# Kernel optimization log

Hardware: AMD Instinct MI355X
Metric: run time of the kernel (lower is better)

The kernel has to match this reference:

```python
import jax, jax.numpy as jnp
import numpy as np

E = 8        # n_experts
H = 1024     # hidden
F = 1024     # ffn intermediate
K = 2        # top_k
B, T = 2, 1024


def setup_inputs() -> dict:
    key = jax.random.key(0)
    k1, k2, k3, k4 = jax.random.split(key, 4)
    return {
        "hidden_states": jax.random.normal(k1, (B, T, H), dtype=jnp.float32),
        "router_weight": jax.random.normal(k2, (E, H), dtype=jnp.float32),
        "gate_up_proj": jax.random.normal(k3, (E, 2 * F, H), dtype=jnp.float32),
        "down_proj": jax.random.normal(k4, (E, H, F), dtype=jnp.float32),
    }


def reference(hidden_states, router_weight, gate_up_proj, down_proj):
    b, t, h_dim = hidden_states.shape
    h = hidden_states.reshape(-1, h_dim)                      # [N, H]

    # Router: logits -> softmax -> top-k -> renormalize (matches FakeFusedRouter)
    logits = h @ router_weight.T                              # [N, E]
    probs = jax.nn.softmax(logits, axis=-1)
    top_v, top_i = jax.lax.top_k(probs, K)                    # [N, K]
    top_v = top_v / top_v.sum(axis=-1, keepdims=True)

    # Combine weights per expert: w[e, n] = sum_k top_v[n,k] * [top_i[n,k]==e]
    combine = (jax.nn.one_hot(top_i, E, dtype=top_v.dtype) * top_v[..., None]).sum(axis=1)  # [N, E]
    combine = combine.T                                       # [E, N]

    # Scan over experts: each expert runs its SwiGLU FFN over all tokens,
    # masked/weighted by combine (zero weight == token not routed there).
    def body(acc, xs):
        gu, dp, w = xs                                        # [2F,H], [H,F], [N]
        gate, up = jnp.split(h @ gu.T, 2, axis=-1)            # [N,F] each
        out = (jax.nn.silu(gate) * up) @ dp.T                 # [N,H]
        return acc + w[:, None] * out, None

    acc0 = jnp.zeros_like(h)
    final, _ = jax.lax.scan(body, acc0, (gate_up_proj, down_proj, combine))
    return final.reshape(b, t, h_dim)
```

## Files before the change

kernel.cpp:

```cpp
#include <hip/hip_runtime.h>


#define NTOK   2048
#define HDIM   1024
#define FDIM   1024
#define NEXP   8
#define NKROWS 4096
#define MAXTILES 40

typedef __attribute__((ext_vector_type(8))) __bf16 bf16x8;
typedef __attribute__((ext_vector_type(4))) float  floatx4;

__device__ __forceinline__ unsigned short f2bf(float x) {
    unsigned int u = __builtin_bit_cast(unsigned int, x);
    u += 0x7FFFu + ((u >> 16) & 1u);
    return (unsigned short)(u >> 16);
}

__device__ __forceinline__ float bf2f(unsigned short v) {
    unsigned int u = (unsigned int)v << 16;
    return __builtin_bit_cast(float, u);
}

__device__ __forceinline__ uint4 pack8(float4 a, float4 b) {
    uint4 o;
    o.x = (unsigned)f2bf(a.x) | ((unsigned)f2bf(a.y) << 16);
    o.y = (unsigned)f2bf(a.z) | ((unsigned)f2bf(a.w) << 16);
    o.z = (unsigned)f2bf(b.x) | ((unsigned)f2bf(b.y) << 16);
    o.w = (unsigned)f2bf(b.z) | ((unsigned)f2bf(b.w) << 16);
    return o;
}

__device__ __forceinline__ void dma16(const void* g, void* l) {
    __builtin_amdgcn_global_load_lds(
        (const __attribute__((address_space(1))) unsigned int*)g,
        (__attribute__((address_space(3))) unsigned int*)l, 16, 0, 0);
}

__global__ __launch_bounds__(256) void k_convert_w(
    const float* __restrict__ gu, const float* __restrict__ dp,
    unsigned short* __restrict__ gubf, unsigned short* __restrict__ dpbf)
{
    int b = blockIdx.x;
    const float* src;
    unsigned short* dst;
    size_t base;
    if (b < 8192) { base = (size_t)b * 2048;          src = gu; dst = gubf; }
    else          { base = (size_t)(b - 8192) * 2048; src = dp; dst = dpbf; }
    size_t i = base + (size_t)threadIdx.x * 8;
    const float4* s = reinterpret_cast<const float4*>(src + i);
    float4 a = s[0], c = s[1];
    *reinterpret_cast<uint4*>(dst + i) = pack8(a, c);
}

__global__ __launch_bounds__(256) void k_router(
    const float* __restrict__ h, const float* __restrict__ rw,
    unsigned short* __restrict__ hbf,
    int* __restrict__ topk_idx, float* __restrict__ topk_w)
{
    const int lane = threadIdx.x & 63;
    const int wave = threadIdx.x >> 6;
    const int n = blockIdx.x * 4 + wave;

    const float4* hp = reinterpret_cast<const float4*>(h + (size_t)n * HDIM);
    uint2* hb = reinterpret_cast<uint2*>(hbf + (size_t)n * HDIM);
    float acc[NEXP];
#pragma unroll
    for (int e = 0; e < NEXP; ++e) acc[e] = 0.f;

#pragma unroll
    for (int i0 = 0; i0 < HDIM / 4; i0 += 64) {
        float4 hv = hp[i0 + lane];
        uint2 o;
        o.x = (unsigned)f2bf(hv.x) | ((unsigned)f2bf(hv.y) << 16);
        o.y = (unsigned)f2bf(hv.z) | ((unsigned)f2bf(hv.w) << 16);
        hb[i0 + lane] = o;
#pragma unroll
        for (int e = 0; e < NEXP; ++e) {
            float4 rv = reinterpret_cast<const float4*>(rw + e * HDIM)[i0 + lane];
            acc[e] += hv.x * rv.x + hv.y * rv.y + hv.z * rv.z + hv.w * rv.w;
        }
    }
#pragma unroll
    for (int e = 0; e < NEXP; ++e) {
#pragma unroll
        for (int off = 32; off > 0; off >>= 1)
            acc[e] += __shfl_xor(acc[e], off);
    }
    if (lane == 0) {
        int i0 = 0; float m0 = acc[0];
        for (int e = 1; e < NEXP; ++e) if (acc[e] > m0) { m0 = acc[e]; i0 = e; }
        int i1 = -1; float m1 = -3.0e38f;
        for (int e = 0; e < NEXP; ++e) if (e != i0 && acc[e] > m1) { m1 = acc[e]; i1 = e; }
        float d  = __expf(m1 - m0);
        float w0 = 1.f / (1.f + d);
        topk_idx[n * 2 + 0] = i0;
        topk_idx[n * 2 + 1] = i1;
        topk_w [n * 2 + 0] = w0;
        topk_w [n * 2 + 1] = 1.f - w0;
    }
}

__global__ __launch_bounds__(256) void k_build_perm(
    const int* __restrict__ topk_idx, const float* __restrict__ topk_w,
    int* __restrict__ offsets, int* __restrict__ perm_slot, float* __restrict__ row_w,
    int* __restrict__ tile_e, int* __restrict__ tile_rt)
{
    __shared__ int cnt[NEXP];
    __shared__ int cur[NEXP];
    __shared__ int off[NEXP + 1];
    const int t = threadIdx.x;
    if (t < NEXP) cnt[t] = 0;
    __syncthreads();
    for (int s = t; s < NKROWS; s += 256) atomicAdd(&cnt[topk_idx[s]], 1);
    __syncthreads();
    if (t == 0) {
        int a = 0;
        for (int e = 0; e < NEXP; ++e) { off[e] = a; a += cnt[e]; cur[e] = off[e]; }
        off[NEXP] = a;
        int nt = 0;
        for (int e = 0; e < NEXP; ++e) {
            int ne = cnt[e];
            for (int r = 0; r * 128 < ne; ++r) { tile_e[nt] = e; tile_rt[nt] = r; ++nt; }
        }
        for (; nt < MAXTILES; ++nt) { tile_e[nt] = -1; tile_rt[nt] = 0; }
    }
    __syncthreads();
    for (int s = t; s < NKROWS; s += 256) {
        int e = topk_idx[s];
        int pos = atomicAdd(&cur[e], 1);
        perm_slot[pos] = s;
        row_w[pos] = topk_w[s];
    }
    if (t < NEXP + 1) offsets[t] = off[t];
}

__global__ __launch_bounds__(256, 2) void k_gemm1(
    const unsigned short* __restrict__ hbf, const unsigned short* __restrict__ gubf,
    const int* __restrict__ offsets, const int* __restrict__ perm_slot,
    const int* __restrict__ tile_e, const int* __restrict__ tile_rt,
    unsigned short* __restrict__ act)
{
    const int e = tile_e[blockIdx.y];
    if (e < 0) return;
    const int rt = tile_rt[blockIdx.y];
    const int off_e = offsets[e];
    const int n_e   = offsets[e + 1] - off_e;
    const int p0 = off_e + rt * 128;
    const int nr = min(128, n_e - rt * 128);
    const int c0 = blockIdx.x * 64;

    __shared__ __align__(16) char smA [2][128 * 128];
    __shared__ __align__(16) char smBg[2][64 * 128];
    __shared__ __align__(16) char smBu[2][64 * 128];
    __shared__ int sTok[128];

    const int t = threadIdx.x;
    const int lane = t & 63;
    const int wv = t >> 6;
    const int wr = wv >> 1, wc = wv & 1;
    if (t < 128) sTok[t] = perm_slot[min(p0 + t, NKROWS - 1)] >> 1;
    __syncthreads();

    const int rin = lane >> 3;
    const int pre = ((lane & 7) << 4) ^ (rin << 4);

    const char* asrc[4];
    int aldo[4];
#pragma unroll
    for (int c = 0; c < 4; ++c) {
        int ch = wv * 4 + c;
        int row = ch * 8 + rin;
        asrc[c] = (const char*)(hbf + (size_t)sTok[row] * HDIM) + pre;
        aldo[c] = ch * 1024;
    }
    const unsigned short* guE = gubf + (size_t)e * (2 * FDIM) * HDIM;
    const char* gsrc[2];
    const char* usrc[2];
    int bldo[2];
#pragma unroll
    for (int c = 0; c < 2; ++c) {
        int ch = wv * 2 + c;
        int col = ch * 8 + rin;
        gsrc[c] = (const char*)(guE + (size_t)(c0 + col) * HDIM) + pre;
        usrc[c] = (const char*)(guE + (size_t)(FDIM + c0 + col) * HDIM) + pre;
        bldo[c] = ch * 1024;
    }

    floatx4 accg[4][2], accu[4][2];
#pragma unroll
    for (int m = 0; m < 4; ++m)
#pragma unroll
        for (int nn = 0; nn < 2; ++nn) { accg[m][nn] = (floatx4)0.f; accu[m][nn] = (floatx4)0.f; }

#define STAGE1(k0, buf)                                                         \
    {                                                                           \
        _Pragma("unroll")                                                       \
        for (int c = 0; c < 4; ++c) dma16(asrc[c] + (size_t)(k0) * 2, smA [buf] + aldo[c]); \
        _Pragma("unroll")                                                       \
        for (int c = 0; c < 2; ++c) dma16(gsrc[c] + (size_t)(k0) * 2, smBg[buf] + bldo[c]); \
        _Pragma("unroll")                                                       \
        for (int c = 0; c < 2; ++c) dma16(usrc[c] + (size_t)(k0) * 2, smBu[buf] + bldo[c]); \
    }

    STAGE1(0, 0);
    STAGE1(64, 1);

    for (int step = 0; step < 16; ++step) {
        if (step < 15) asm volatile("s_waitcnt vmcnt(8)" ::: "memory");
        else           asm volatile("s_waitcnt vmcnt(0)" ::: "memory");
        __builtin_amdgcn_s_barrier();
        __builtin_amdgcn_sched_barrier(0);
        const int cur = step & 1;
#pragma unroll
        for (int kk = 0; kk < 2; ++kk) {
            const int kA = kk * 64 + (lane >> 4) * 16;
            bf16x8 a[4], fg[2], fu[2];
#pragma unroll
            for (int m = 0; m < 4; ++m) {
                int row = wr * 64 + m * 16 + (lane & 15);
                a[m] = *reinterpret_cast<const bf16x8*>(&smA[cur][row * 128 + (kA ^ ((row & 7) << 4))]);
            }
#pragma unroll
            for (int nn = 0; nn < 2; ++nn) {
                int cc = wc * 32 + nn * 16 + (lane & 15);
                int ad = cc * 128 + (kA ^ ((cc & 7) << 4));
                fg[nn] = *reinterpret_cast<const bf16x8*>(&smBg[cur][ad]);
                fu[nn] = *reinterpret_cast<const bf16x8*>(&smBu[cur][ad]);
            }
#pragma unroll
            for (int m = 0; m < 4; ++m)
#pragma unroll
                for (int nn = 0; nn < 2; ++nn) {
                    accg[m][nn] = __builtin_amdgcn_mfma_f32_16x16x32_bf16(a[m], fg[nn], accg[m][nn], 0, 0, 0);
                    accu[m][nn] = __builtin_amdgcn_mfma_f32_16x16x32_bf16(a[m], fu[nn], accu[m][nn], 0, 0, 0);
                }
        }
        __builtin_amdgcn_sched_barrier(0);
        __builtin_amdgcn_s_barrier();
        if (step < 14) STAGE1((step + 2) * 64, cur);
    }
#undef STAGE1

#pragma unroll
    for (int m = 0; m < 4; ++m)
#pragma unroll
        for (int nn = 0; nn < 2; ++nn)
#pragma unroll
            for (int j = 0; j < 4; ++j) {
                int rr = wr * 64 + m * 16 + ((lane >> 4) << 2) + j;
                if (rr < nr) {
                    int f = c0 + wc * 32 + nn * 16 + (lane & 15);
                    float gg = accg[m][nn][j];
                    float uu = accu[m][nn][j];
                    float s = gg / (1.f + __expf(-gg));
                    act[(size_t)(p0 + rr) * FDIM + f] = f2bf(s * uu);
                }
            }
}

__global__ __launch_bounds__(256, 2) void k_gemm2(
    const unsigned short* __restrict__ act, const unsigned short* __restrict__ dpbf,
    const int* __restrict__ offsets, const int* __restrict__ perm_slot,
    const int* __restrict__ tile_e, const int* __restrict__ tile_rt,
    const float* __restrict__ row_w, unsigned short* __restrict__ partial)
{
    const int e = tile_e[blockIdx.y];
    if (e < 0) return;
    const int rt = tile_rt[blockIdx.y];
    const int off_e = offsets[e];
    const int n_e   = offsets[e + 1] - off_e;
    const int p0 = off_e + rt * 128;
    const int nr = min(128, n_e - rt * 128);
    const int c0 = blockIdx.x * 128;

    __shared__ __align__(16) char smA[2][128 * 128];
    __shared__ __align__(16) char smB[2][128 * 128];
    __shared__ int   sSlot[128];
    __shared__ float sW[128];

    const int t = threadIdx.x;
    const int lane = t & 63;
    const int wv = t >> 6;
    const int wr = wv >> 1, wc = wv & 1;
    if (t < 128) {
        int p = min(p0 + t, NKROWS - 1);
        sSlot[t] = perm_slot[p];
        sW[t]    = row_w[p];
    }
    __syncthreads();

    const int rin = lane >> 3;
    const int pre = ((lane & 7) << 4) ^ (rin << 4);

    const char* asrc[4];
    int aldo[4];
#pragma unroll
    for (int c = 0; c < 4; ++c) {
        int ch = wv * 4 + c;
        int row = ch * 8 + rin;
        int p = min(p0 + row, NKROWS - 1);
        asrc[c] = (const char*)(act + (size_t)p * FDIM) + pre;
        aldo[c] = ch * 1024;
    }
    const unsigned short* dpE = dpbf + (size_t)e * HDIM * FDIM;
    const char* bsrc[4];
    int bldo[4];
#pragma unroll
    for (int c = 0; c < 4; ++c) {
        int ch = wv * 4 + c;
        int col = ch * 8 + rin;
        bsrc[c] = (const char*)(dpE + (size_t)(c0 + col) * FDIM) + pre;
        bldo[c] = ch * 1024;
    }

    floatx4 acc[4][4];
#pragma unroll
    for (int m = 0; m < 4; ++m)
#pragma unroll
        for (int nn = 0; nn < 4; ++nn) acc[m][nn] = (floatx4)0.f;

#define STAGE2(k0, buf)                                                         \
    {                                                                           \
        _Pragma("unroll")                                                       \
        for (int c = 0; c < 4; ++c) dma16(asrc[c] + (size_t)(k0) * 2, smA[buf] + aldo[c]); \
        _Pragma("unroll")                                                       \
        for (int c = 0; c < 4; ++c) dma16(bsrc[c] + (size_t)(k0) * 2, smB[buf] + bldo[c]); \
    }

    STAGE2(0, 0);
    STAGE2(64, 1);

    for (int step = 0; step < 16; ++step) {
        if (step < 15) asm volatile("s_waitcnt vmcnt(8)" ::: "memory");
        else           asm volatile("s_waitcnt vmcnt(0)" ::: "memory");
        __builtin_amdgcn_s_barrier();
        __builtin_amdgcn_sched_barrier(0);
        const int cur = step & 1;
#pragma unroll
        for (int kk = 0; kk < 2; ++kk) {
            const int kA = kk * 64 + (lane >> 4) * 16;
            bf16x8 a[4], fb[4];
#pragma unroll
            for (int m = 0; m < 4; ++m) {
                int row = wr * 64 + m * 16 + (lane & 15);
                a[m] = *reinterpret_cast<const bf16x8*>(&smA[cur][row * 128 + (kA ^ ((row & 7) << 4))]);
            }
#pragma unroll
            for (int nn = 0; nn < 4; ++nn) {
                int cc = wc * 64 + nn * 16 + (lane & 15);
                fb[nn] = *reinterpret_cast<const bf16x8*>(&smB[cur][cc * 128 + (kA ^ ((cc & 7) << 4))]);
            }
#pragma unroll
            for (int m = 0; m < 4; ++m)
#pragma unroll
                for (int nn = 0; nn < 4; ++nn)
                    acc[m][nn] = __builtin_amdgcn_mfma_f32_16x16x32_bf16(a[m], fb[nn], acc[m][nn], 0, 0, 0);
        }
        __builtin_amdgcn_sched_barrier(0);
        __builtin_amdgcn_s_barrier();
        if (step < 14) STAGE2((step + 2) * 64, cur);
    }
#undef STAGE2

#pragma unroll
    for (int m = 0; m < 4; ++m)
#pragma unroll
        for (int nn = 0; nn < 4; ++nn)
#pragma unroll
            for (int j = 0; j < 4; ++j) {
                int rr = wr * 64 + m * 16 + ((lane >> 4) << 2) + j;
                if (rr < nr) {
                    int hcol = c0 + wc * 64 + nn * 16 + (lane & 15);
                    partial[(size_t)sSlot[rr] * HDIM + hcol] = f2bf(sW[rr] * acc[m][nn][j]);
                }
            }
}

__global__ __launch_bounds__(256) void k_combine(
    const unsigned short* __restrict__ partial, float* __restrict__ out)
{
    int gid = blockIdx.x * 256 + threadIdx.x;
    int n = gid >> 7;
    int r = gid & 127;
    uint4 a = reinterpret_cast<const uint4*>(partial + (size_t)(2 * n) * HDIM)[r];
    uint4 b = reinterpret_cast<const uint4*>(partial + (size_t)(2 * n + 1) * HDIM)[r];
    float4 o0, o1;
    o0.x = bf2f(a.x & 0xFFFF) + bf2f(b.x & 0xFFFF);
    o0.y = bf2f(a.x >> 16)    + bf2f(b.x >> 16);
    o0.z = bf2f(a.y & 0xFFFF) + bf2f(b.y & 0xFFFF);
    o0.w = bf2f(a.y >> 16)    + bf2f(b.y >> 16);
    o1.x = bf2f(a.z & 0xFFFF) + bf2f(b.z & 0xFFFF);
    o1.y = bf2f(a.z >> 16)    + bf2f(b.z >> 16);
    o1.z = bf2f(a.w & 0xFFFF) + bf2f(b.w & 0xFFFF);
    o1.w = bf2f(a.w >> 16)    + bf2f(b.w >> 16);
    float4* op = reinterpret_cast<float4*>(out + (size_t)n * HDIM + r * 8);
    op[0] = o0;
    op[1] = o1;
}

extern "C" void kernel_launch(void* const* d_in, const int* in_sizes, int n_in,
                              void* d_out, int out_size, void* d_ws, size_t ws_size,
                              hipStream_t stream)
{
    const float* h  = (const float*)d_in[0];
    const float* rw = (const float*)d_in[1];
    const float* gu = (const float*)d_in[2];
    const float* dp = (const float*)d_in[3];
    float* out = (float*)d_out;

    char* ws = (char*)d_ws;
    int*            topk_idx  = (int*)   (ws + 0);
    float*          topk_w    = (float*) (ws + 16384);
    int*            offsets   = (int*)   (ws + 32768);
    int*            tile_e    = (int*)   (ws + 33024);
    int*            tile_rt   = (int*)   (ws + 33280);
    int*            perm_slot = (int*)   (ws + 36864);
    float*          row_w     = (float*) (ws + 53248);
    unsigned short* hbf       = (unsigned short*)(ws + (1u  << 20));
    unsigned short* partial   = (unsigned short*)(ws + (1u  << 20));
    unsigned short* act       = (unsigned short*)(ws + (9u  << 20));
    unsigned short* gubf      = (unsigned short*)(ws + (17u << 20));
    unsigned short* dpbf      = (unsigned short*)(ws + (49u << 20));

    hipLaunchKernelGGL(k_convert_w,  dim3(12288), dim3(256), 0, stream, gu, dp, gubf, dpbf);
    hipLaunchKernelGGL(k_router,     dim3(512),   dim3(256), 0, stream, h, rw, hbf, topk_idx, topk_w);
    hipLaunchKernelGGL(k_build_perm, dim3(1),     dim3(256), 0, stream, topk_idx, topk_w, offsets, perm_slot, row_w, tile_e, tile_rt);
    hipLaunchKernelGGL(k_gemm1,      dim3(16, MAXTILES), dim3(256), 0, stream, hbf, gubf, offsets, perm_slot, tile_e, tile_rt, act);
    hipLaunchKernelGGL(k_gemm2,      dim3(8,  MAXTILES), dim3(256), 0, stream, act, dpbf, offsets, perm_slot, tile_e, tile_rt, row_w, partial);
    hipLaunchKernelGGL(k_combine,    dim3(1024), dim3(256), 0, stream, partial, out);
}
```

Baseline: 109.1 us.

## Fuse weight conversion into router and gemm1, expert-interleaved tile queues

The weight-conversion kernel is split up. The gate_up conversion now shares a launch with the router, and the down_proj conversion is appended as extra blocks of the gemm1 launch, so that conversion overlaps the first GEMM and one launch is dropped. The 2D grid with a tile_e/tile_rt list is replaced by per-expert queues that encode expert, row tile and column tile, read in an expert-interleaved order (bid&7 selects the expert) so that block scheduling spreads work across experts. The risk is more early-exit padding blocks, and dp conversion blocks competing with GEMM blocks for CUs.

Result: slower. 158.4 us (+45.2%).

```diff
diff --git a/kernel.cpp b/kernel.cpp
--- a/kernel.cpp
+++ b/kernel.cpp
@@ -6,7 +6,8 @@
 #define FDIM   1024
 #define NEXP   8
 #define NKROWS 4096
-#define MAXTILES 40
+#define Q1LEN  160
+#define Q2LEN  80
 
 typedef __attribute__((ext_vector_type(8))) __bf16 bf16x8;
 typedef __attribute__((ext_vector_type(4))) float  floatx4;
@@ -37,30 +38,23 @@
         (__attribute__((address_space(3))) unsigned int*)l, 16, 0, 0);
 }
 
-__global__ __launch_bounds__(256) void k_convert_w(
-    const float* __restrict__ gu, const float* __restrict__ dp,
-    unsigned short* __restrict__ gubf, unsigned short* __restrict__ dpbf)
-{
-    int b = blockIdx.x;
-    const float* src;
-    unsigned short* dst;
-    size_t base;
-    if (b < 8192) { base = (size_t)b * 2048;          src = gu; dst = gubf; }
-    else          { base = (size_t)(b - 8192) * 2048; src = dp; dst = dpbf; }
-    size_t i = base + (size_t)threadIdx.x * 8;
-    const float4* s = reinterpret_cast<const float4*>(src + i);
-    float4 a = s[0], c = s[1];
-    *reinterpret_cast<uint4*>(dst + i) = pack8(a, c);
-}
-
-__global__ __launch_bounds__(256) void k_router(
+__global__ __launch_bounds__(256) void k_pre(
+    const float* __restrict__ gu, unsigned short* __restrict__ gubf,
     const float* __restrict__ h, const float* __restrict__ rw,
     unsigned short* __restrict__ hbf,
     int* __restrict__ topk_idx, float* __restrict__ topk_w)
 {
+    const int b = blockIdx.x;
+    if (b < 8192) {
+        size_t i = (size_t)b * 2048 + (size_t)threadIdx.x * 8;
+        const float4* s = reinterpret_cast<const float4*>(gu + i);
+        float4 a = s[0], c = s[1];
+        *reinterpret_cast<uint4*>(gubf + i) = pack8(a, c);
+        return;
+    }
     const int lane = threadIdx.x & 63;
     const int wave = threadIdx.x >> 6;
-    const int n = blockIdx.x * 4 + wave;
+    const int n = (b - 8192) * 4 + wave;
 
     const float4* hp = reinterpret_cast<const float4*>(h + (size_t)n * HDIM);
     uint2* hb = reinterpret_cast<uint2*>(hbf + (size_t)n * HDIM);
@@ -104,7 +98,7 @@
 __global__ __launch_bounds__(256) void k_build_perm(
     const int* __restrict__ topk_idx, const float* __restrict__ topk_w,
     int* __restrict__ offsets, int* __restrict__ perm_slot, float* __restrict__ row_w,
-    int* __restrict__ tile_e, int* __restrict__ tile_rt)
+    int* __restrict__ q1, int* __restrict__ q2)
 {
     __shared__ int cnt[NEXP];
     __shared__ int cur[NEXP];
@@ -118,12 +112,19 @@
         int a = 0;
         for (int e = 0; e < NEXP; ++e) { off[e] = a; a += cnt[e]; cur[e] = off[e]; }
         off[NEXP] = a;
-        int nt = 0;
         for (int e = 0; e < NEXP; ++e) {
-            int ne = cnt[e];
-            for (int r = 0; r * 128 < ne; ++r) { tile_e[nt] = e; tile_rt[nt] = r; ++nt; }
+            int rts = (cnt[e] + 127) >> 7;
+            int k = 0;
+            for (int col = 0; col < 16; ++col)
+                for (int r = 0; r < rts; ++r)
+                    if (k < Q1LEN) q1[e * Q1LEN + k++] = e | (r << 4) | (col << 9);
+            for (; k < Q1LEN; ++k) q1[e * Q1LEN + k] = -1;
+            k = 0;
+            for (int col = 0; col < 8; ++col)
+                for (int r = 0; r < rts; ++r)
+                    if (k < Q2LEN) q2[e * Q2LEN + k++] = e | (r << 4) | (col << 9);
+            for (; k < Q2LEN; ++k) q2[e * Q2LEN + k] = -1;
         }
-        for (; nt < MAXTILES; ++nt) { tile_e[nt] = -1; tile_rt[nt] = 0; }
     }
     __syncthreads();
     for (int s = t; s < NKROWS; s += 256) {
@@ -138,17 +139,27 @@
 __global__ __launch_bounds__(256, 2) void k_gemm1(
     const unsigned short* __restrict__ hbf, const unsigned short* __restrict__ gubf,
     const int* __restrict__ offsets, const int* __restrict__ perm_slot,
-    const int* __restrict__ tile_e, const int* __restrict__ tile_rt,
+    const int* __restrict__ q1,
+    const float* __restrict__ dp, unsigned short* __restrict__ dpbf,
     unsigned short* __restrict__ act)
 {
-    const int e = tile_e[blockIdx.y];
-    if (e < 0) return;
-    const int rt = tile_rt[blockIdx.y];
+    const int bid = blockIdx.x;
+    if (bid >= 8 * Q1LEN) {
+        size_t i = (size_t)(bid - 8 * Q1LEN) * 2048 + (size_t)threadIdx.x * 8;
+        const float4* s = reinterpret_cast<const float4*>(dp + i);
+        float4 a = s[0], c = s[1];
+        *reinterpret_cast<uint4*>(dpbf + i) = pack8(a, c);
+        return;
+    }
+    const int q = q1[(bid & 7) * Q1LEN + (bid >> 3)];
+    if (q < 0) return;
+    const int e  = q & 15;
+    const int rt = (q >> 4) & 31;
+    const int c0 = (q >> 9) * 64;
     const int off_e = offsets[e];
     const int n_e   = offsets[e + 1] - off_e;
     const int p0 = off_e + rt * 128;
     const int nr = min(128, n_e - rt * 128);
-    const int c0 = blockIdx.x * 64;
 
     __shared__ __align__(16) char smA [2][128 * 128];
     __shared__ __align__(16) char smBg[2][64 * 128];
@@ -262,17 +273,19 @@
 __global__ __launch_bounds__(256, 2) void k_gemm2(
     const unsigned short* __restrict__ act, const unsigned short* __restrict__ dpbf,
     const int* __restrict__ offsets, const int* __restrict__ perm_slot,
-    const int* __restrict__ tile_e, const int* __restrict__ tile_rt,
+    const int* __restrict__ q2,
     const float* __restrict__ row_w, unsigned short* __restrict__ partial)
 {
-    const int e = tile_e[blockIdx.y];
-    if (e < 0) return;
-    const int rt = tile_rt[blockIdx.y];
+    const int bid = blockIdx.x;
+    const int q = q2[(bid & 7) * Q2LEN + (bid >> 3)];
+    if (q < 0) return;
+    const int e  = q & 15;
+    const int rt = (q >> 4) & 31;
+    const int c0 = (q >> 9) * 128;
     const int off_e = offsets[e];
     const int n_e   = offsets[e + 1] - off_e;
     const int p0 = off_e + rt * 128;
     const int nr = min(128, n_e - rt * 128);
-    const int c0 = blockIdx.x * 128;
 
     __shared__ __align__(16) char smA[2][128 * 128];
     __shared__ __align__(16) char smB[2][128 * 128];
@@ -413,20 +426,19 @@
     int*            topk_idx  = (int*)   (ws + 0);
     float*          topk_w    = (float*) (ws + 16384);
     int*            offsets   = (int*)   (ws + 32768);
-    int*            tile_e    = (int*)   (ws + 33024);
-    int*            tile_rt   = (int*)   (ws + 33280);
     int*            perm_slot = (int*)   (ws + 36864);
     float*          row_w     = (float*) (ws + 53248);
+    int*            q1        = (int*)   (ws + 69632);
+    int*            q2        = (int*)   (ws + 74752);
     unsigned short* hbf       = (unsigned short*)(ws + (1u  << 20));
     unsigned short* partial   = (unsigned short*)(ws + (1u  << 20));
     unsigned short* act       = (unsigned short*)(ws + (9u  << 20));
     unsigned short* gubf      = (unsigned short*)(ws + (17u << 20));
     unsigned short* dpbf      = (unsigned short*)(ws + (49u << 20));
 
-    hipLaunchKernelGGL(k_convert_w,  dim3(12288), dim3(256), 0, stream, gu, dp, gubf, dpbf);
-    hipLaunchKernelGGL(k_router,     dim3(512),   dim3(256), 0, stream, h, rw, hbf, topk_idx, topk_w);
-    hipLaunchKernelGGL(k_build_perm, dim3(1),     dim3(256), 0, stream, topk_idx, topk_w, offsets, perm_slot, row_w, tile_e, tile_rt);
-    hipLaunchKernelGGL(k_gemm1,      dim3(16, MAXTILES), dim3(256), 0, stream, hbf, gubf, offsets, perm_slot, tile_e, tile_rt, act);
-    hipLaunchKernelGGL(k_gemm2,      dim3(8,  MAXTILES), dim3(256), 0, stream, act, dpbf, offsets, perm_slot, tile_e, tile_rt, row_w, partial);
-    hipLaunchKernelGGL(k_combine,    dim3(1024), dim3(256), 0, stream, partial, out);
-}
+    hipLaunchKernelGGL(k_pre,        dim3(8704),            dim3(256), 0, stream, gu, gubf, h, rw, hbf, topk_idx, topk_w);
+    hipLaunchKernelGGL(k_build_perm, dim3(1),               dim3(256), 0, stream, topk_idx, topk_w, offsets, perm_slot, row_w, q1, q2);
+    hipLaunchKernelGGL(k_gemm1,      dim3(8 * Q1LEN + 4096), dim3(256), 0, stream, hbf, gubf, offsets, perm_slot, q1, dp, dpbf, act);
+    hipLaunchKernelGGL(k_gemm2,      dim3(8 * Q2LEN),        dim3(256), 0, stream, act, dpbf, offsets, perm_slot, q2, row_w, partial);
+    hipLaunchKernelGGL(k_combine,    dim3(1024),            dim3(256), 0, stream, partial, out);
+}
```
